# Kernel tuning notes

Hardware: AMD Instinct MI355X
Metric: run time of the kernel (lower is better)

The kernel has to match this reference:

```python
import jax, jax.numpy as jnp
import numpy as np

K = 64        # top-k from init_kwargs
TAU = 1.0     # temperature at step=0: tau_start*(1-0) + tau_end*0


def setup_inputs() -> dict:
    key = jax.random.key(0)
    k1, k2 = jax.random.split(key)
    B, N = 2048, 8192
    logits = jax.random.normal(k1, (B, N), dtype=jnp.float32)
    # gumbels = -log(Exp(1)) == standard Gumbel noise
    gumbel_noise = jax.random.gumbel(k2, (B, N), dtype=jnp.float32)
    return {"logits": logits, "gumbel_noise": gumbel_noise}


def reference(logits, gumbel_noise):
    # training path of GumbelTopK (step=0 -> tau=TAU, hard=True)
    g = (logits + gumbel_noise) / TAU                       # [B, N]
    order = jnp.argsort(-g, axis=-1)                        # descending sort order
    sorted_g = jnp.take_along_axis(g, order, axis=-1)
    cumsum = jnp.cumsum(jax.nn.softmax(sorted_g, axis=-1), axis=-1)
    mask = (cumsum <= K).astype(sorted_g.dtype)             # NB: faithful to source (<= k)
    sorted_y = mask * jax.nn.softmax(sorted_g / TAU, axis=-1)
    # scatter back to original positions == gather by inverse permutation
    inv = jnp.argsort(order, axis=-1)
    y = jnp.take_along_axis(sorted_y, inv, axis=-1)         # [B, N]
    # hard straight-through: one-hot-k of y
    k = min(K, y.shape[-1])
    _, idx = jax.lax.top_k(y, k)                            # [B, k]
    rows = jnp.arange(y.shape[0])[:, None]
    y_hard = jnp.zeros_like(y).at[rows, idx].set(1.0)
    return jax.lax.stop_gradient(y_hard - y) + y
```

## Files before the change

### kernel.cpp

```cpp
#include <hip/hip_runtime.h>

constexpr int N = 8192;
constexpr int K = 64;
constexpr int THREADS = 256;
constexpr int WAVES = THREADS / 64;
constexpr int VEC = N / THREADS / 4;
constexpr int SEGCAP = 256;

__device__ __forceinline__ unsigned orderable(float f) {
    unsigned x = __float_as_uint(f);
    return (x & 0x80000000u) ? ~x : (x | 0x80000000u);
}

__global__ __launch_bounds__(THREADS, 8)
void gumbel_topk_onehot(const float* __restrict__ logits,
                        const float* __restrict__ noise,
                        float* __restrict__ out)
{
    __shared__ unsigned long long seg[WAVES * SEGCAP];
    __shared__ unsigned long long dst[WAVES * SEGCAP];
    __shared__ unsigned counts[WAVES];
    __shared__ unsigned wavesum[WAVES];
    __shared__ unsigned sel_bin, sel_kth, sel_cnt;

    unsigned* hist = (unsigned*)seg;

    const int tid  = threadIdx.x;
    const int lane = tid & 63;
    const int wave = tid >> 6;
    const long long row = blockIdx.x;

    const float4* lrow = (const float4*)(logits + row * (long long)N);
    const float4* nrow = (const float4*)(noise  + row * (long long)N);
    float4* orow = (float4*)(out + row * (long long)N);

    const unsigned T0 = orderable(4.0f);
    const unsigned long long lt = (1ull << lane) - 1ull;

    unsigned wcnt = 0;

#define EMIT(kk, elem)                                                        \
    {                                                                         \
        bool p = (kk) > T0;                                                   \
        unsigned long long m = __ballot(p);                                   \
        if (p) {                                                              \
            unsigned pos = wcnt + (unsigned)__popcll(m & lt);                 \
            if (pos < (unsigned)SEGCAP)                                       \
                seg[wave * SEGCAP + pos] =                                    \
                    ((unsigned long long)(kk) << 32) |                        \
                    (unsigned long long)(unsigned)(N - 1 - (elem));           \
        }                                                                     \
        wcnt += (unsigned)__popcll(m);                                        \
    }

#pragma unroll
    for (int i = 0; i < VEC; ++i) {
        int idx = tid + i * THREADS;
        float4 a = lrow[idx];
        float4 b = nrow[idx];
        unsigned k0 = orderable(a.x + b.x);
        unsigned k1 = orderable(a.y + b.y);
        unsigned k2 = orderable(a.z + b.z);
        unsigned k3 = orderable(a.w + b.w);
        orow[idx] = make_float4(0.f, 0.f, 0.f, 0.f);
        EMIT(k0, 4 * idx + 0)
        EMIT(k1, 4 * idx + 1)
        EMIT(k2, 4 * idx + 2)
        EMIT(k3, 4 * idx + 3)
    }
#undef EMIT
    if (lane == 0) counts[wave] = wcnt;
    __syncthreads();

    const unsigned c0 = counts[0], c1 = counts[1], c2 = counts[2], c3 = counts[3];
    const unsigned n = c0 + c1 + c2 + c3;
    const bool ok = (n >= (unsigned)K) &&
                    (c0 <= SEGCAP) && (c1 <= SEGCAP) && (c2 <= SEGCAP) && (c3 <= SEGCAP);

    if (ok) {
        const unsigned offs[WAVES] = {0u, c0, c0 + c1, c0 + c1 + c2};
        const unsigned cws[WAVES]  = {c0, c1, c2, c3};
#pragma unroll
        for (int w = 0; w < WAVES; ++w)
            for (unsigned l = tid; l < cws[w]; l += THREADS)
                dst[offs[w] + l] = seg[w * SEGCAP + l];
        __syncthreads();

        for (unsigned t = tid; t < n; t += THREADS) {
            unsigned long long ct = dst[t];
            unsigned rank = 0;
            for (unsigned j = 0; j < n; ++j)
                rank += (dst[j] > ct) ? 1u : 0u;
            if (rank < (unsigned)K) {
                unsigned elem = (unsigned)(N - 1) - (unsigned)(ct & 0xFFFFFFFFull);
                out[row * (long long)N + elem] = 1.0f;
            }
        }
        return;
    }

    unsigned kth = K;

#define SELECT_BIN(BPT)                                                      \
    {                                                                        \
        unsigned p = 0;                                                      \
        _Pragma("unroll")                                                    \
        for (int j = 0; j < (BPT); ++j) p += hist[tid * (BPT) + j];          \
        unsigned s = p;                                                      \
        _Pragma("unroll")                                                    \
        for (int off = 1; off < 64; off <<= 1) {                             \
            unsigned v = __shfl_down(s, off);                                \
            if (lane + off < 64) s += v;                                     \
        }                                                                    \
        if (lane == 0) wavesum[wave] = s;                                    \
        __syncthreads();                                                     \
        unsigned S = s;                                                      \
        _Pragma("unroll")                                                    \
        for (int w = 0; w < WAVES; ++w) if (w > wave) S += wavesum[w];       \
        unsigned Snext = S - p;                                              \
        if (S >= kth && Snext < kth) {                                       \
            unsigned cum = Snext;                                            \
            for (int j = (BPT) - 1; j >= 0; --j) {                           \
                unsigned c = hist[tid * (BPT) + j];                          \
                if (cum + c >= kth) {                                        \
                    sel_bin = (unsigned)(tid * (BPT) + j);                   \
                    sel_kth = kth - cum;                                     \
                    sel_cnt = c;                                             \
                    break;                                                   \
                }                                                            \
                cum += c;                                                    \
            }                                                                \
        }                                                                    \
        __syncthreads();                                                     \
    }

    {
        uint4 z = make_uint4(0, 0, 0, 0);
        for (int i = tid; i < 512; i += THREADS) ((uint4*)hist)[i] = z;
    }
    __syncthreads();
#pragma unroll
    for (int i = 0; i < VEC; ++i) {
        int idx = tid + i * THREADS;
        float4 a = lrow[idx];
        float4 b = nrow[idx];
        atomicAdd(&hist[orderable(a.x + b.x) >> 21], 1u);
        atomicAdd(&hist[orderable(a.y + b.y) >> 21], 1u);
        atomicAdd(&hist[orderable(a.z + b.z) >> 21], 1u);
        atomicAdd(&hist[orderable(a.w + b.w) >> 21], 1u);
    }
    __syncthreads();
    SELECT_BIN(8)
    const unsigned b1 = sel_bin;
    kth = sel_kth;
    __syncthreads();

    {
        uint4 z = make_uint4(0, 0, 0, 0);
        for (int i = tid; i < 512; i += THREADS) ((uint4*)hist)[i] = z;
    }
    __syncthreads();
#pragma unroll
    for (int i = 0; i < VEC; ++i) {
        int idx = tid + i * THREADS;
        float4 a = lrow[idx];
        float4 b = nrow[idx];
        unsigned k0 = orderable(a.x + b.x), k1 = orderable(a.y + b.y);
        unsigned k2 = orderable(a.z + b.z), k3 = orderable(a.w + b.w);
        if ((k0 >> 21) == b1) atomicAdd(&hist[(k0 >> 10) & 0x7FFu], 1u);
        if ((k1 >> 21) == b1) atomicAdd(&hist[(k1 >> 10) & 0x7FFu], 1u);
        if ((k2 >> 21) == b1) atomicAdd(&hist[(k2 >> 10) & 0x7FFu], 1u);
        if ((k3 >> 21) == b1) atomicAdd(&hist[(k3 >> 10) & 0x7FFu], 1u);
    }
    __syncthreads();
    SELECT_BIN(8)
    const unsigned b2 = sel_bin;
    kth = sel_kth;
    __syncthreads();

    {
        uint4 z = make_uint4(0, 0, 0, 0);
        for (int i = tid; i < 256; i += THREADS) ((uint4*)hist)[i] = z;
    }
    __syncthreads();
    {
        const unsigned pfx = (b1 << 11) | b2;
#pragma unroll
        for (int i = 0; i < VEC; ++i) {
            int idx = tid + i * THREADS;
            float4 a = lrow[idx];
            float4 b = nrow[idx];
            unsigned k0 = orderable(a.x + b.x), k1 = orderable(a.y + b.y);
            unsigned k2 = orderable(a.z + b.z), k3 = orderable(a.w + b.w);
            if ((k0 >> 10) == pfx) atomicAdd(&hist[k0 & 0x3FFu], 1u);
            if ((k1 >> 10) == pfx) atomicAdd(&hist[k1 & 0x3FFu], 1u);
            if ((k2 >> 10) == pfx) atomicAdd(&hist[k2 & 0x3FFu], 1u);
            if ((k3 >> 10) == pfx) atomicAdd(&hist[k3 & 0x3FFu], 1u);
        }
    }
    __syncthreads();
    SELECT_BIN(4)
    const unsigned b3      = sel_bin;
    const unsigned take_eq = sel_kth;
    const unsigned c_eq    = sel_cnt;

    const unsigned T = (b1 << 21) | (b2 << 10) | b3;
    const bool fast = (take_eq == c_eq);

#pragma unroll
    for (int i = 0; i < VEC; ++i) {
        int idx = tid + i * THREADS;
        float4 a = lrow[idx];
        float4 b = nrow[idx];
        unsigned k0 = orderable(a.x + b.x), k1 = orderable(a.y + b.y);
        unsigned k2 = orderable(a.z + b.z), k3 = orderable(a.w + b.w);
        float4 o;
        o.x = (k0 > T || (fast && k0 == T)) ? 1.0f : 0.0f;
        o.y = (k1 > T || (fast && k1 == T)) ? 1.0f : 0.0f;
        o.z = (k2 > T || (fast && k2 == T)) ? 1.0f : 0.0f;
        o.w = (k3 > T || (fast && k3 == T)) ? 1.0f : 0.0f;
        orow[idx] = o;
    }

    if (!fast) {
        __syncthreads();
        if (tid == 0) {
            const float* lf = logits + row * (long long)N;
            const float* nf = noise  + row * (long long)N;
            float* of = out + row * (long long)N;
            unsigned c = 0;
            for (int i = 0; i < N; ++i) {
                if (orderable(lf[i] + nf[i]) == T) {
                    of[i] = 1.0f;
                    if (++c == take_eq) break;
                }
            }
        }
    }
#undef SELECT_BIN
}

extern "C" void kernel_launch(void* const* d_in, const int* in_sizes, int n_in,
                              void* d_out, int out_size, void* d_ws, size_t ws_size,
                              hipStream_t stream) {
    const float* logits = (const float*)d_in[0];
    const float* noise  = (const float*)d_in[1];
    float* out = (float*)d_out;
    const int rows = in_sizes[0] / N;
    gumbel_topk_onehot<<<rows, THREADS, 0, stream>>>(logits, noise, out);
}
```

Baseline: 182.8 us.

## Batch row loads, hoist zero stores, and make candidate LDS writes branchless

The zeroing stores for the output row are hoisted into a separate loop ahead of the scan. The scan loop now issues four float4 loads per input before processing them, so more memory requests are in flight. The candidate emit path drops its divergent branch: every lane writes unconditionally, and non-candidates go to a per-lane dump slot in a padded shared buffer. This costs more shared-memory writes and more registers, which may reduce occupancy.

```diff
diff --git a/kernel.cpp b/kernel.cpp
--- a/kernel.cpp
+++ b/kernel.cpp
@@ -6,6 +6,7 @@
 constexpr int WAVES = THREADS / 64;
 constexpr int VEC = N / THREADS / 4;
 constexpr int SEGCAP = 256;
+constexpr int SEGSTRIDE = SEGCAP + 64;
 
 __device__ __forceinline__ unsigned orderable(float f) {
     unsigned x = __float_as_uint(f);
@@ -17,7 +18,7 @@
                         const float* __restrict__ noise,
                         float* __restrict__ out)
 {
-    __shared__ unsigned long long seg[WAVES * SEGCAP];
+    __shared__ unsigned long long seg[WAVES * SEGSTRIDE];
     __shared__ unsigned long long dst[WAVES * SEGCAP];
     __shared__ unsigned counts[WAVES];
     __shared__ unsigned wavesum[WAVES];
@@ -36,6 +37,11 @@
 
     const unsigned T0 = orderable(4.0f);
     const unsigned long long lt = (1ull << lane) - 1ull;
+    const unsigned dump = (unsigned)SEGCAP + (unsigned)lane;
+
+#pragma unroll
+    for (int i = 0; i < VEC; ++i)
+        orow[tid + i * THREADS] = make_float4(0.f, 0.f, 0.f, 0.f);
 
     unsigned wcnt = 0;
 
@@ -43,32 +49,42 @@
     {                                                                         \
         bool p = (kk) > T0;                                                   \
         unsigned long long m = __ballot(p);                                   \
-        if (p) {                                                              \
-            unsigned pos = wcnt + (unsigned)__popcll(m & lt);                 \
-            if (pos < (unsigned)SEGCAP)                                       \
-                seg[wave * SEGCAP + pos] =                                    \
-                    ((unsigned long long)(kk) << 32) |                        \
-                    (unsigned long long)(unsigned)(N - 1 - (elem));           \
-        }                                                                     \
+        unsigned pos = wcnt + (unsigned)__popcll(m & lt);                     \
+        unsigned slot = (p && pos < (unsigned)SEGCAP) ? pos : dump;           \
+        seg[wave * SEGSTRIDE + slot] =                                        \
+            ((unsigned long long)(kk) << 32) |                                \
+            (unsigned long long)(unsigned)(N - 1 - (elem));                   \
         wcnt += (unsigned)__popcll(m);                                        \
     }
 
-#pragma unroll
-    for (int i = 0; i < VEC; ++i) {
-        int idx = tid + i * THREADS;
-        float4 a = lrow[idx];
-        float4 b = nrow[idx];
-        unsigned k0 = orderable(a.x + b.x);
-        unsigned k1 = orderable(a.y + b.y);
-        unsigned k2 = orderable(a.z + b.z);
-        unsigned k3 = orderable(a.w + b.w);
-        orow[idx] = make_float4(0.f, 0.f, 0.f, 0.f);
-        EMIT(k0, 4 * idx + 0)
-        EMIT(k1, 4 * idx + 1)
-        EMIT(k2, 4 * idx + 2)
-        EMIT(k3, 4 * idx + 3)
-    }
+#define EMIT4(va, vb, i4)                                                     \
+    {                                                                         \
+        unsigned k0 = orderable((va).x + (vb).x);                             \
+        unsigned k1 = orderable((va).y + (vb).y);                             \
+        unsigned k2 = orderable((va).z + (vb).z);                             \
+        unsigned k3 = orderable((va).w + (vb).w);                             \
+        EMIT(k0, 4 * (i4) + 0)                                                \
+        EMIT(k1, 4 * (i4) + 1)                                                \
+        EMIT(k2, 4 * (i4) + 2)                                                \
+        EMIT(k3, 4 * (i4) + 3)                                                \
+    }
+
+#pragma unroll
+    for (int c = 0; c < VEC; c += 4) {
+        int i0 = tid + (c + 0) * THREADS;
+        int i1 = tid + (c + 1) * THREADS;
+        int i2 = tid + (c + 2) * THREADS;
+        int i3 = tid + (c + 3) * THREADS;
+        float4 a0 = lrow[i0], a1 = lrow[i1], a2 = lrow[i2], a3 = lrow[i3];
+        float4 b0 = nrow[i0], b1 = nrow[i1], b2 = nrow[i2], b3 = nrow[i3];
+        EMIT4(a0, b0, i0)
+        EMIT4(a1, b1, i1)
+        EMIT4(a2, b2, i2)
+        EMIT4(a3, b3, i3)
+    }
+#undef EMIT4
 #undef EMIT
+
     if (lane == 0) counts[wave] = wcnt;
     __syncthreads();
 
@@ -83,7 +99,7 @@
 #pragma unroll
         for (int w = 0; w < WAVES; ++w)
             for (unsigned l = tid; l < cws[w]; l += THREADS)
-                dst[offs[w] + l] = seg[w * SEGCAP + l];
+                dst[offs[w] + l] = seg[w * SEGSTRIDE + l];
         __syncthreads();
 
         for (unsigned t = tid; t < n; t += THREADS) {
```

Measured after the change: 182.3 us. About the same (-0.3%).
